# Optimization experiments

Hardware: AMD Instinct MI355X
Metric: run time of the kernel (lower is better)

## Reference

```python
import jax, jax.numpy as jnp
import numpy as np

KERNEL_MUL = 2.0
KERNEL_NUM = 5


def _mmd_channel(s, t):
    """Multi-bandwidth Gaussian-kernel MMD for one channel. s,t: [B, D]."""
    B = s.shape[0]
    total = jnp.concatenate([s, t], axis=0)            # [2B, D]
    sq = jnp.sum(total * total, axis=1)                # [2B]
    # ||xi - xj||^2 via Gram identity (avoids [2B,2B,D] intermediate)
    L2 = sq[:, None] + sq[None, :] - 2.0 * (total @ total.T)  # [2B, 2B]
    n = 2 * B
    # torch uses L2_distance.data -> bandwidth is detached
    bandwidth = jax.lax.stop_gradient(jnp.sum(L2)) / (n * n - n)
    bandwidth = bandwidth / (KERNEL_MUL ** (KERNEL_NUM // 2))
    bws = bandwidth * (KERNEL_MUL ** jnp.arange(KERNEL_NUM, dtype=s.dtype))  # [K_num]
    kernels = jnp.sum(jnp.exp(-L2[None, :, :] / bws[:, None, None]), axis=0)  # [2B, 2B]
    XX = kernels[:B, :B]
    YY = kernels[B:, B:]
    XY = kernels[:B, B:]
    YX = kernels[B:, :B]
    return jnp.mean(XX + YY - XY - YX)


def setup_inputs() -> dict:
    key = jax.random.key(0)
    k1, k2 = jax.random.split(key)
    B, K, H, W = 128, 21, 64, 64
    source = jax.random.normal(k1, (B, K, H, W), dtype=jnp.float32)
    target = jax.random.normal(k2, (B, K, H, W), dtype=jnp.float32)
    return {"source": source, "target": target}


def reference(source, target):
    B, K = source.shape[0], source.shape[1]
    s = source.reshape(B, K, -1)  # [B, K, D]
    t = target.reshape(B, K, -1)
    per_channel = jax.vmap(_mmd_channel, in_axes=(1, 1))(s, t)  # [K]
    return jnp.sum(per_channel) / K
```

## Files before the change

### kernel.cpp

```cpp
#include <hip/hip_runtime.h>
#include <hip/hip_bf16.h>
#include <stdint.h>

typedef __attribute__((ext_vector_type(4))) float f32x4;
typedef __attribute__((ext_vector_type(8))) short bf16x8;
typedef __attribute__((ext_vector_type(4))) uint32_t u32x4;

#define NCH 21
#define NROW 256
#define DIM 4096
#define BMP 128
#define BK 64
#define LDSS 72
#define NTILE 10

__device__ const int g_TI[NTILE] = {0, 0, 0, 0, 1, 1, 1, 2, 2, 3};
__device__ const int g_TJ[NTILE] = {0, 1, 2, 3, 1, 2, 3, 2, 3, 3};

__device__ __forceinline__ uint32_t pack_bf2(float x, float y) {
  __hip_bfloat162 h = __float22bfloat162_rn(float2{x, y});
  union { __hip_bfloat162 h; uint32_t u; } c;
  c.h = h;
  return c.u;
}

__global__ __launch_bounds__(512) void gram_kernel(
    const float* __restrict__ src, const float* __restrict__ tgt,
    float* __restrict__ Gp, int kshift, int kchunk) {
  const int P = 1 << kshift;
  const int NG = NCH << kshift;
  const int q = NG >> 3, r8 = NG & 7;
  const int x = blockIdx.x & 7;
  const int slot = blockIdx.x >> 3;
  const int cnt = q + (x < r8 ? 1 : 0);
  if (slot >= cnt * 3) return;
  const int gbase = (x < r8) ? x * (q + 1) : r8 * (q + 1) + (x - r8) * q;
  const int gi = slot / 3;
  const int bt = slot - gi * 3;
  const int g = gbase + gi;
  const int ch = g >> kshift;
  const int ks = g & (P - 1);
  const int kbase = ks * kchunk;
  const int row_base = (bt == 1) ? 128 : 0;
  const int col_base = (bt == 0) ? 0 : 128;
  const bool isdiag = (bt != 2);
  const int tid = threadIdx.x;
  const int lane = tid & 63;

  __shared__ __attribute__((aligned(16))) ushort As[BMP * LDSS];
  __shared__ __attribute__((aligned(16))) ushort Bs[BMP * LDSS];

  f32x4 acc[2][4];
#pragma unroll
  for (int m = 0; m < 2; ++m)
#pragma unroll
    for (int n = 0; n < 4; ++n)
      acc[m][n] = (f32x4){0.f, 0.f, 0.f, 0.f};

  const int wave = tid >> 6;
  const int wr = (wave >> 1) * 32;
  const int wc = (wave & 1) * 64;

  const int r0 = tid >> 3;
  const int c8 = (tid & 7) * 8;
  const float* Ab = row_base ? tgt : src;
  const float* Bb = col_base ? tgt : src;
  const float* ap[2];
  const float* bp[2];
#pragma unroll
  for (int p = 0; p < 2; ++p) {
    ap[p] = Ab + ((size_t)(r0 + p * 64) * NCH + ch) * DIM + c8;
    bp[p] = Bb + ((size_t)(r0 + p * 64) * NCH + ch) * DIM + c8;
  }

  f32x4 va[2][2], vb[2][2];
#pragma unroll
  for (int p = 0; p < 2; ++p) {
    va[p][0] = *reinterpret_cast<const f32x4*>(ap[p] + kbase);
    va[p][1] = *reinterpret_cast<const f32x4*>(ap[p] + kbase + 4);
    if (!isdiag) {
      vb[p][0] = *reinterpret_cast<const f32x4*>(bp[p] + kbase);
      vb[p][1] = *reinterpret_cast<const f32x4*>(bp[p] + kbase + 4);
    }
  }

  const int kend = kbase + kchunk;
  for (int k0 = kbase; k0 < kend; k0 += BK) {
    __syncthreads();
#pragma unroll
    for (int p = 0; p < 2; ++p) {
      u32x4 wa;
      wa.x = pack_bf2(va[p][0].x, va[p][0].y);
      wa.y = pack_bf2(va[p][0].z, va[p][0].w);
      wa.z = pack_bf2(va[p][1].x, va[p][1].y);
      wa.w = pack_bf2(va[p][1].z, va[p][1].w);
      *reinterpret_cast<u32x4*>(&As[(r0 + p * 64) * LDSS + c8]) = wa;
      if (!isdiag) {
        u32x4 wb;
        wb.x = pack_bf2(vb[p][0].x, vb[p][0].y);
        wb.y = pack_bf2(vb[p][0].z, vb[p][0].w);
        wb.z = pack_bf2(vb[p][1].x, vb[p][1].y);
        wb.w = pack_bf2(vb[p][1].z, vb[p][1].w);
        *reinterpret_cast<u32x4*>(&Bs[(r0 + p * 64) * LDSS + c8]) = wb;
      }
    }
    if (k0 + BK < kend) {
#pragma unroll
      for (int p = 0; p < 2; ++p) {
        va[p][0] = *reinterpret_cast<const f32x4*>(ap[p] + k0 + BK);
        va[p][1] = *reinterpret_cast<const f32x4*>(ap[p] + k0 + BK + 4);
        if (!isdiag) {
          vb[p][0] = *reinterpret_cast<const f32x4*>(bp[p] + k0 + BK);
          vb[p][1] = *reinterpret_cast<const f32x4*>(bp[p] + k0 + BK + 4);
        }
      }
    }
    asm volatile("s_waitcnt lgkmcnt(0)" ::: "memory");
    __builtin_amdgcn_s_barrier();
    asm volatile("" ::: "memory");

    const ushort* Bsrc = isdiag ? As : Bs;
#pragma unroll
    for (int kk = 0; kk < 2; ++kk) {
      const int kb = kk * 32 + (lane >> 4) * 8;
      bf16x8 a[2], b[4];
#pragma unroll
      for (int m = 0; m < 2; ++m)
        a[m] = *reinterpret_cast<const bf16x8*>(
            &As[(wr + m * 16 + (lane & 15)) * LDSS + kb]);
#pragma unroll
      for (int n = 0; n < 4; ++n)
        b[n] = *reinterpret_cast<const bf16x8*>(
            &Bsrc[(wc + n * 16 + (lane & 15)) * LDSS + kb]);
#pragma unroll
      for (int m = 0; m < 2; ++m)
#pragma unroll
        for (int n = 0; n < 4; ++n)
          acc[m][n] = __builtin_amdgcn_mfma_f32_16x16x32_bf16(a[m], b[n],
                                                              acc[m][n], 0, 0, 0);
    }
  }

  float* gp = Gp + (size_t)(ch * P + ks) * (NROW * NROW);
#pragma unroll
  for (int m = 0; m < 2; ++m)
#pragma unroll
    for (int n = 0; n < 4; ++n) {
      const int grow = row_base + wr + m * 16 + ((lane >> 4) << 2);
      const int gcol = col_base + wc + n * 16 + (lane & 15);
      if ((grow >> 6) > (gcol >> 6)) continue;
#pragma unroll
      for (int j = 0; j < 4; ++j)
        gp[(size_t)(grow + j) * NROW + gcol] = acc[m][n][j];
    }
}

__device__ __forceinline__ float block_sum256(float v, float* sm) {
#pragma unroll
  for (int o = 32; o > 0; o >>= 1) v += __shfl_down(v, o, 64);
  const int lane = threadIdx.x & 63;
  const int w = threadIdx.x >> 6;
  if (lane == 0) sm[w] = v;
  __syncthreads();
  float r = 0.f;
  if (threadIdx.x == 0) r = sm[0] + sm[1] + sm[2] + sm[3];
  __syncthreads();
  return r;
}

__global__ __launch_bounds__(256) void foldsum_kernel(
    const f32x4* __restrict__ Gp, f32x4* __restrict__ Gf,
    float* __restrict__ sums, int P) {
  const int t = blockIdx.x;
  const int ch = blockIdx.y;
  const int ti = g_TI[t], tj = g_TJ[t];
  const bool isdiag = (ti == tj);
  const int tid = threadIdx.x;
  float s = 0.f, tr = 0.f;
#pragma unroll
  for (int i = 0; i < 4; ++i) {
    const int idx4 = tid * 4 + i;
    const int rrow = idx4 >> 4;
    const int c4 = idx4 & 15;
    const int base_v = (ti * 64 + rrow) * 64 + tj * 16 + c4;
    f32x4 v = Gp[(size_t)(ch * P) * 16384 + base_v];
    for (int p = 1; p < P; ++p) v += Gp[(size_t)(ch * P + p) * 16384 + base_v];
    Gf[(size_t)ch * 16384 + base_v] = v;
    s += (v.x + v.y) + (v.z + v.w);
    if (isdiag) {
      const int cb = c4 * 4;
#pragma unroll
      for (int e = 0; e < 4; ++e)
        if (cb + e == rrow) tr += v[e];
    }
  }
  __shared__ float sm[4];
  float sG = block_sum256(s, sm);
  float sT = block_sum256(tr, sm);
  if (tid == 0) {
    sums[ch * 20 + t] = sG;
    if (isdiag) sums[ch * 20 + 10 + ti] = sT;
  }
}

__global__ __launch_bounds__(256) void mmd_kernel(const float* __restrict__ Gf,
                                                  const float* __restrict__ sums,
                                                  float* __restrict__ partial) {
  const int t = blockIdx.x;
  const int ch = blockIdx.y;
  const int ti = g_TI[t], tj = g_TJ[t];
  const int tid = threadIdx.x;
  const float* g = Gf + (size_t)ch * (NROW * NROW);

  const float* sc = sums + ch * 20;
  float sumG = 0.f;
#pragma unroll
  for (int k = 0; k < NTILE; ++k)
    sumG += (g_TI[k] == g_TJ[k] ? 1.f : 2.f) * sc[k];
  const float trace = (sc[10] + sc[11]) + (sc[12] + sc[13]);
  const float sumL2 = 2.f * NROW * trace - 2.f * sumG;
  const float bw = sumL2 / (float)(NROW * NROW - NROW) * 0.25f;
  float inv[5];
#pragma unroll
  for (int a = 0; a < 5; ++a) inv[a] = -1.f / (bw * (float)(1 << a));

  __shared__ float dA[64], dB[64];
  if (tid < 64) dA[tid] = g[(size_t)(ti * 64 + tid) * (NROW + 1)];
  else if (tid < 128) dB[tid - 64] = g[(size_t)(tj * 64 + (tid - 64)) * (NROW + 1)];
  __syncthreads();

  const int col = tid & 63;
  const int qq = tid >> 6;
  const float dj = dB[col];
  float acc = 0.f;
#pragma unroll 4
  for (int it = 0; it < 16; ++it) {
    const int r = it * 4 + qq;
    const float L2 = dA[r] + dj - 2.f * g[(size_t)(ti * 64 + r) * NROW + tj * 64 + col];
    float kv = 0.f;
#pragma unroll
    for (int a = 0; a < 5; ++a) kv += __expf(L2 * inv[a]);
    acc += kv;
  }
  __shared__ float sm[4];
  float tot = block_sum256(acc, sm);
  if (tid == 0) {
    float w = (ti == tj) ? 1.f : 2.f;
    float sgn = ((ti >= 2) == (tj >= 2)) ? 1.f : -1.f;
    partial[ch * NTILE + t] = tot * w * sgn;
  }
}

__global__ __launch_bounds__(256) void final_kernel(const float* __restrict__ partial,
                                                    float* __restrict__ out) {
  const int tid = threadIdx.x;
  float v = (tid < NCH * NTILE) ? partial[tid] : 0.f;
  __shared__ float sm[4];
  float tot = block_sum256(v, sm);
  if (tid == 0) out[0] = tot * (1.f / (NCH * 128.f * 128.f));
}

extern "C" void kernel_launch(void* const* d_in, const int* in_sizes, int n_in,
                              void* d_out, int out_size, void* d_ws, size_t ws_size,
                              hipStream_t stream) {
  const float* src = (const float*)d_in[0];
  const float* tgt = (const float*)d_in[1];
  float* out = (float*)d_out;
  const size_t GSZ = (size_t)NROW * NROW;

  int kshift = 0;
  if (ws_size >= (NCH * 9 * GSZ + 512) * sizeof(float)) kshift = 3;
  else if (ws_size >= (NCH * 5 * GSZ + 512) * sizeof(float)) kshift = 2;
  else if (ws_size >= (NCH * 3 * GSZ + 512) * sizeof(float)) kshift = 1;
  const int P = 1 << kshift;

  float* Gp = (float*)d_ws;
  float* Gf = (P > 1) ? Gp + (size_t)NCH * P * GSZ : Gp;
  float* sums = Gf + (size_t)NCH * GSZ;
  float* partial = sums + NCH * 20;

  const int NG = NCH * P;
  const int q = NG / 8, r8 = NG % 8;
  const int grid = 8 * (q + (r8 ? 1 : 0)) * 3;

  gram_kernel<<<dim3(grid), 512, 0, stream>>>(src, tgt, Gp, kshift, DIM >> kshift);
  foldsum_kernel<<<dim3(NTILE, NCH), 256, 0, stream>>>((const f32x4*)Gp,
                                                       (f32x4*)Gf, sums, P);
  mmd_kernel<<<dim3(NTILE, NCH), 256, 0, stream>>>(Gf, sums, partial);
  final_kernel<<<1, 256, 0, stream>>>(partial, out);
}
```

Baseline: 45.91 us.

## Double-buffer global prefetch registers and allow a 16-way K split

The Gram kernel's K loop is unrolled by two and keeps two register sets of prefetched fp32 data, so global loads are issued two BK steps ahead of the MFMA work that consumes them. The host also gains a kshift=4 option, splitting K into 16 chunks when the workspace is large enough, which raises block count but makes the fold-sum kernel read twice as many partial Gram matrices. The extra register buffers raise VGPR pressure. The loop assumes each K chunk holds an even number of BK steps, which holds for the chunk sizes in use.

```diff
diff --git a/kernel.cpp b/kernel.cpp
--- a/kernel.cpp
+++ b/kernel.cpp
@@ -22,6 +22,48 @@
   union { __hip_bfloat162 h; uint32_t u; } c;
   c.h = h;
   return c.u;
+}
+
+struct StageCtx {
+  const float* ap[2];
+  const float* bp[2];
+  bool isdiag;
+  int r0, c8, kend;
+};
+
+__device__ __forceinline__ void fill_slot(const StageCtx& cx, f32x4 (&va)[2][2],
+                                          f32x4 (&vb)[2][2], int k) {
+#pragma unroll
+  for (int p = 0; p < 2; ++p) {
+    va[p][0] = *reinterpret_cast<const f32x4*>(cx.ap[p] + k);
+    va[p][1] = *reinterpret_cast<const f32x4*>(cx.ap[p] + k + 4);
+    if (!cx.isdiag) {
+      vb[p][0] = *reinterpret_cast<const f32x4*>(cx.bp[p] + k);
+      vb[p][1] = *reinterpret_cast<const f32x4*>(cx.bp[p] + k + 4);
+    }
+  }
+}
+
+__device__ __forceinline__ void stage_slot(const StageCtx& cx, ushort* As,
+                                           ushort* Bs, f32x4 (&va)[2][2],
+                                           f32x4 (&vb)[2][2]) {
+#pragma unroll
+  for (int p = 0; p < 2; ++p) {
+    u32x4 wa;
+    wa.x = pack_bf2(va[p][0].x, va[p][0].y);
+    wa.y = pack_bf2(va[p][0].z, va[p][0].w);
+    wa.z = pack_bf2(va[p][1].x, va[p][1].y);
+    wa.w = pack_bf2(va[p][1].z, va[p][1].w);
+    *reinterpret_cast<u32x4*>(&As[(cx.r0 + p * 64) * LDSS + cx.c8]) = wa;
+    if (!cx.isdiag) {
+      u32x4 wb;
+      wb.x = pack_bf2(vb[p][0].x, vb[p][0].y);
+      wb.y = pack_bf2(vb[p][0].z, vb[p][0].w);
+      wb.z = pack_bf2(vb[p][1].x, vb[p][1].y);
+      wb.w = pack_bf2(vb[p][1].z, vb[p][1].w);
+      *reinterpret_cast<u32x4*>(&Bs[(cx.r0 + p * 64) * LDSS + cx.c8]) = wb;
+    }
+  }
 }
 
 __global__ __launch_bounds__(512) void gram_kernel(
@@ -43,7 +85,6 @@
   const int kbase = ks * kchunk;
   const int row_base = (bt == 1) ? 128 : 0;
   const int col_base = (bt == 0) ? 0 : 128;
-  const bool isdiag = (bt != 2);
   const int tid = threadIdx.x;
   const int lane = tid & 63;
 
@@ -61,83 +102,86 @@
   const int wr = (wave >> 1) * 32;
   const int wc = (wave & 1) * 64;
 
-  const int r0 = tid >> 3;
-  const int c8 = (tid & 7) * 8;
-  const float* Ab = row_base ? tgt : src;
-  const float* Bb = col_base ? tgt : src;
-  const float* ap[2];
-  const float* bp[2];
-#pragma unroll
-  for (int p = 0; p < 2; ++p) {
-    ap[p] = Ab + ((size_t)(r0 + p * 64) * NCH + ch) * DIM + c8;
-    bp[p] = Bb + ((size_t)(r0 + p * 64) * NCH + ch) * DIM + c8;
-  }
-
-  f32x4 va[2][2], vb[2][2];
-#pragma unroll
-  for (int p = 0; p < 2; ++p) {
-    va[p][0] = *reinterpret_cast<const f32x4*>(ap[p] + kbase);
-    va[p][1] = *reinterpret_cast<const f32x4*>(ap[p] + kbase + 4);
-    if (!isdiag) {
-      vb[p][0] = *reinterpret_cast<const f32x4*>(bp[p] + kbase);
-      vb[p][1] = *reinterpret_cast<const f32x4*>(bp[p] + kbase + 4);
-    }
-  }
-
-  const int kend = kbase + kchunk;
-  for (int k0 = kbase; k0 < kend; k0 += BK) {
-    __syncthreads();
+  StageCtx cx;
+  cx.isdiag = (bt != 2);
+  cx.r0 = tid >> 3;
+  cx.c8 = (tid & 7) * 8;
+  cx.kend = kbase + kchunk;
+  {
+    const float* Ab = row_base ? tgt : src;
+    const float* Bb = col_base ? tgt : src;
 #pragma unroll
     for (int p = 0; p < 2; ++p) {
-      u32x4 wa;
-      wa.x = pack_bf2(va[p][0].x, va[p][0].y);
-      wa.y = pack_bf2(va[p][0].z, va[p][0].w);
-      wa.z = pack_bf2(va[p][1].x, va[p][1].y);
-      wa.w = pack_bf2(va[p][1].z, va[p][1].w);
-      *reinterpret_cast<u32x4*>(&As[(r0 + p * 64) * LDSS + c8]) = wa;
-      if (!isdiag) {
-        u32x4 wb;
-        wb.x = pack_bf2(vb[p][0].x, vb[p][0].y);
-        wb.y = pack_bf2(vb[p][0].z, vb[p][0].w);
-        wb.z = pack_bf2(vb[p][1].x, vb[p][1].y);
-        wb.w = pack_bf2(vb[p][1].z, vb[p][1].w);
-        *reinterpret_cast<u32x4*>(&Bs[(r0 + p * 64) * LDSS + c8]) = wb;
-      }
-    }
-    if (k0 + BK < kend) {
-#pragma unroll
-      for (int p = 0; p < 2; ++p) {
-        va[p][0] = *reinterpret_cast<const f32x4*>(ap[p] + k0 + BK);
-        va[p][1] = *reinterpret_cast<const f32x4*>(ap[p] + k0 + BK + 4);
-        if (!isdiag) {
-          vb[p][0] = *reinterpret_cast<const f32x4*>(bp[p] + k0 + BK);
-          vb[p][1] = *reinterpret_cast<const f32x4*>(bp[p] + k0 + BK + 4);
-        }
-      }
-    }
+      cx.ap[p] = Ab + ((size_t)(cx.r0 + p * 64) * NCH + ch) * DIM + cx.c8;
+      cx.bp[p] = Bb + ((size_t)(cx.r0 + p * 64) * NCH + ch) * DIM + cx.c8;
+    }
+  }
+
+  f32x4 vaA[2][2], vbA[2][2], vaB[2][2], vbB[2][2];
+  fill_slot(cx, vaA, vbA, kbase);
+  fill_slot(cx, vaB, vbB, kbase + BK);
+
+  for (int k0 = kbase; k0 < cx.kend; k0 += 2 * BK) {
+    asm volatile("s_waitcnt lgkmcnt(0)" ::: "memory");
+    __builtin_amdgcn_s_barrier();
+    stage_slot(cx, As, Bs, vaA, vbA);
+    if (k0 + 2 * BK < cx.kend) fill_slot(cx, vaA, vbA, k0 + 2 * BK);
     asm volatile("s_waitcnt lgkmcnt(0)" ::: "memory");
     __builtin_amdgcn_s_barrier();
     asm volatile("" ::: "memory");
 
-    const ushort* Bsrc = isdiag ? As : Bs;
-#pragma unroll
-    for (int kk = 0; kk < 2; ++kk) {
-      const int kb = kk * 32 + (lane >> 4) * 8;
-      bf16x8 a[2], b[4];
-#pragma unroll
-      for (int m = 0; m < 2; ++m)
-        a[m] = *reinterpret_cast<const bf16x8*>(
-            &As[(wr + m * 16 + (lane & 15)) * LDSS + kb]);
-#pragma unroll
-      for (int n = 0; n < 4; ++n)
-        b[n] = *reinterpret_cast<const bf16x8*>(
-            &Bsrc[(wc + n * 16 + (lane & 15)) * LDSS + kb]);
-#pragma unroll
-      for (int m = 0; m < 2; ++m)
+    {
+      const ushort* Bsrc = cx.isdiag ? As : Bs;
+#pragma unroll
+      for (int kk = 0; kk < 2; ++kk) {
+        const int kb = kk * 32 + (lane >> 4) * 8;
+        bf16x8 a[2], b[4];
+#pragma unroll
+        for (int m = 0; m < 2; ++m)
+          a[m] = *reinterpret_cast<const bf16x8*>(
+              &As[(wr + m * 16 + (lane & 15)) * LDSS + kb]);
 #pragma unroll
         for (int n = 0; n < 4; ++n)
-          acc[m][n] = __builtin_amdgcn_mfma_f32_16x16x32_bf16(a[m], b[n],
-                                                              acc[m][n], 0, 0, 0);
+          b[n] = *reinterpret_cast<const bf16x8*>(
+              &Bsrc[(wc + n * 16 + (lane & 15)) * LDSS + kb]);
+#pragma unroll
+        for (int m = 0; m < 2; ++m)
+#pragma unroll
+          for (int n = 0; n < 4; ++n)
+            acc[m][n] = __builtin_amdgcn_mfma_f32_16x16x32_bf16(a[m], b[n],
+                                                                acc[m][n], 0, 0, 0);
+      }
+    }
+
+    asm volatile("s_waitcnt lgkmcnt(0)" ::: "memory");
+    __builtin_amdgcn_s_barrier();
+    stage_slot(cx, As, Bs, vaB, vbB);
+    if (k0 + 3 * BK < cx.kend) fill_slot(cx, vaB, vbB, k0 + 3 * BK);
+    asm volatile("s_waitcnt lgkmcnt(0)" ::: "memory");
+    __builtin_amdgcn_s_barrier();
+    asm volatile("" ::: "memory");
+
+    {
+      const ushort* Bsrc = cx.isdiag ? As : Bs;
+#pragma unroll
+      for (int kk = 0; kk < 2; ++kk) {
+        const int kb = kk * 32 + (lane >> 4) * 8;
+        bf16x8 a[2], b[4];
+#pragma unroll
+        for (int m = 0; m < 2; ++m)
+          a[m] = *reinterpret_cast<const bf16x8*>(
+              &As[(wr + m * 16 + (lane & 15)) * LDSS + kb]);
+#pragma unroll
+        for (int n = 0; n < 4; ++n)
+          b[n] = *reinterpret_cast<const bf16x8*>(
+              &Bsrc[(wc + n * 16 + (lane & 15)) * LDSS + kb]);
+#pragma unroll
+        for (int m = 0; m < 2; ++m)
+#pragma unroll
+          for (int n = 0; n < 4; ++n)
+            acc[m][n] = __builtin_amdgcn_mfma_f32_16x16x32_bf16(a[m], b[n],
+                                                                acc[m][n], 0, 0, 0);
+      }
     }
   }
 
@@ -269,7 +313,8 @@
   const size_t GSZ = (size_t)NROW * NROW;
 
   int kshift = 0;
-  if (ws_size >= (NCH * 9 * GSZ + 512) * sizeof(float)) kshift = 3;
+  if (ws_size >= (NCH * 17 * GSZ + 512) * sizeof(float)) kshift = 4;
+  else if (ws_size >= (NCH * 9 * GSZ + 512) * sizeof(float)) kshift = 3;
   else if (ws_size >= (NCH * 5 * GSZ + 512) * sizeof(float)) kshift = 2;
   else if (ws_size >= (NCH * 3 * GSZ + 512) * sizeof(float)) kshift = 1;
   const int P = 1 << kshift;
```

Result: slower. 83.61 us (+82.1%).

## Restructure gram kernel global loads: wider BK, row-contiguous wave loads, no prefetch

Applied to the files above, without the earlier changes.

The gram kernel now uses a K-tile of 128 instead of 64. Each wave loads 16 rows, with 32 lanes covering a contiguous 512-byte span of one row, so every load instruction issues 8 independent float4 loads per operand. The register-prefetch double buffering is replaced by load-then-store within each iteration, with a barrier added at the end of each iteration, and a launch-bounds occupancy hint is added. The goal is better global coalescing and more memory parallelism per instruction with fewer barriers per unit of K. The cost is losing overlap of global loads with MFMA work, and the LDS footprint roughly doubles, which may limit occupancy.

```diff
diff --git a/kernel.cpp b/kernel.cpp
--- a/kernel.cpp
+++ b/kernel.cpp
@@ -4,14 +4,12 @@
 
 typedef __attribute__((ext_vector_type(4))) float f32x4;
 typedef __attribute__((ext_vector_type(8))) short bf16x8;
-typedef __attribute__((ext_vector_type(4))) uint32_t u32x4;
 
 #define NCH 21
 #define NROW 256
 #define DIM 4096
-#define BMP 128
-#define BK 64
-#define LDSS 72
+#define BK 128
+#define LDSS2 132
 #define NTILE 10
 
 __device__ const int g_TI[NTILE] = {0, 0, 0, 0, 1, 1, 1, 2, 2, 3};
@@ -24,7 +22,7 @@
   return c.u;
 }
 
-__global__ __launch_bounds__(512) void gram_kernel(
+__global__ __launch_bounds__(512, 4) void gram_kernel(
     const float* __restrict__ src, const float* __restrict__ tgt,
     float* __restrict__ Gp, int kshift, int kchunk) {
   const int P = 1 << kshift;
@@ -46,9 +44,10 @@
   const bool isdiag = (bt != 2);
   const int tid = threadIdx.x;
   const int lane = tid & 63;
-
-  __shared__ __attribute__((aligned(16))) ushort As[BMP * LDSS];
-  __shared__ __attribute__((aligned(16))) ushort Bs[BMP * LDSS];
+  const int w = tid >> 6;
+
+  __shared__ __attribute__((aligned(16))) ushort As[128 * LDSS2];
+  __shared__ __attribute__((aligned(16))) ushort Bs[128 * LDSS2];
 
   f32x4 acc[2][4];
 #pragma unroll
@@ -57,62 +56,46 @@
     for (int n = 0; n < 4; ++n)
       acc[m][n] = (f32x4){0.f, 0.f, 0.f, 0.f};
 
-  const int wave = tid >> 6;
-  const int wr = (wave >> 1) * 32;
-  const int wc = (wave & 1) * 64;
-
-  const int r0 = tid >> 3;
-  const int c8 = (tid & 7) * 8;
+  const int wr = (w >> 1) * 32;
+  const int wc = (w & 1) * 64;
+
+  const int subrow = lane >> 5;
+  const int kf = (lane & 31) * 4;
   const float* Ab = row_base ? tgt : src;
   const float* Bb = col_base ? tgt : src;
-  const float* ap[2];
-  const float* bp[2];
-#pragma unroll
-  for (int p = 0; p < 2; ++p) {
-    ap[p] = Ab + ((size_t)(r0 + p * 64) * NCH + ch) * DIM + c8;
-    bp[p] = Bb + ((size_t)(r0 + p * 64) * NCH + ch) * DIM + c8;
-  }
-
-  f32x4 va[2][2], vb[2][2];
-#pragma unroll
-  for (int p = 0; p < 2; ++p) {
-    va[p][0] = *reinterpret_cast<const f32x4*>(ap[p] + kbase);
-    va[p][1] = *reinterpret_cast<const f32x4*>(ap[p] + kbase + 4);
+  const float* apr[8];
+  const float* bpr[8];
+#pragma unroll
+  for (int p = 0; p < 8; ++p) {
+    const int row = w * 16 + 2 * p + subrow;
+    apr[p] = Ab + ((size_t)row * NCH + ch) * DIM + kbase + kf;
+    bpr[p] = Bb + ((size_t)row * NCH + ch) * DIM + kbase + kf;
+  }
+  const int lw0 = (w * 16 + subrow) * LDSS2 + kf;
+
+  const int nk = kchunk / BK;
+
+  for (int it = 0; it < nk; ++it) {
+    const int ko = it * BK;
+    f32x4 v[8];
+#pragma unroll
+    for (int p = 0; p < 8; ++p) v[p] = *reinterpret_cast<const f32x4*>(apr[p] + ko);
+#pragma unroll
+    for (int p = 0; p < 8; ++p) {
+      uint2 wv;
+      wv.x = pack_bf2(v[p].x, v[p].y);
+      wv.y = pack_bf2(v[p].z, v[p].w);
+      *reinterpret_cast<uint2*>(&As[lw0 + 2 * p * LDSS2]) = wv;
+    }
     if (!isdiag) {
-      vb[p][0] = *reinterpret_cast<const f32x4*>(bp[p] + kbase);
-      vb[p][1] = *reinterpret_cast<const f32x4*>(bp[p] + kbase + 4);
-    }
-  }
-
-  const int kend = kbase + kchunk;
-  for (int k0 = kbase; k0 < kend; k0 += BK) {
-    __syncthreads();
-#pragma unroll
-    for (int p = 0; p < 2; ++p) {
-      u32x4 wa;
-      wa.x = pack_bf2(va[p][0].x, va[p][0].y);
-      wa.y = pack_bf2(va[p][0].z, va[p][0].w);
-      wa.z = pack_bf2(va[p][1].x, va[p][1].y);
-      wa.w = pack_bf2(va[p][1].z, va[p][1].w);
-      *reinterpret_cast<u32x4*>(&As[(r0 + p * 64) * LDSS + c8]) = wa;
-      if (!isdiag) {
-        u32x4 wb;
-        wb.x = pack_bf2(vb[p][0].x, vb[p][0].y);
-        wb.y = pack_bf2(vb[p][0].z, vb[p][0].w);
-        wb.z = pack_bf2(vb[p][1].x, vb[p][1].y);
-        wb.w = pack_bf2(vb[p][1].z, vb[p][1].w);
-        *reinterpret_cast<u32x4*>(&Bs[(r0 + p * 64) * LDSS + c8]) = wb;
-      }
-    }
-    if (k0 + BK < kend) {
-#pragma unroll
-      for (int p = 0; p < 2; ++p) {
-        va[p][0] = *reinterpret_cast<const f32x4*>(ap[p] + k0 + BK);
-        va[p][1] = *reinterpret_cast<const f32x4*>(ap[p] + k0 + BK + 4);
-        if (!isdiag) {
-          vb[p][0] = *reinterpret_cast<const f32x4*>(bp[p] + k0 + BK);
-          vb[p][1] = *reinterpret_cast<const f32x4*>(bp[p] + k0 + BK + 4);
-        }
+#pragma unroll
+      for (int p = 0; p < 8; ++p) v[p] = *reinterpret_cast<const f32x4*>(bpr[p] + ko);
+#pragma unroll
+      for (int p = 0; p < 8; ++p) {
+        uint2 wv;
+        wv.x = pack_bf2(v[p].x, v[p].y);
+        wv.y = pack_bf2(v[p].z, v[p].w);
+        *reinterpret_cast<uint2*>(&Bs[lw0 + 2 * p * LDSS2]) = wv;
       }
     }
     asm volatile("s_waitcnt lgkmcnt(0)" ::: "memory");
@@ -121,17 +104,17 @@
 
     const ushort* Bsrc = isdiag ? As : Bs;
 #pragma unroll
-    for (int kk = 0; kk < 2; ++kk) {
+    for (int kk = 0; kk < 4; ++kk) {
       const int kb = kk * 32 + (lane >> 4) * 8;
       bf16x8 a[2], b[4];
 #pragma unroll
       for (int m = 0; m < 2; ++m)
         a[m] = *reinterpret_cast<const bf16x8*>(
-            &As[(wr + m * 16 + (lane & 15)) * LDSS + kb]);
+            &As[(wr + m * 16 + (lane & 15)) * LDSS2 + kb]);
 #pragma unroll
       for (int n = 0; n < 4; ++n)
         b[n] = *reinterpret_cast<const bf16x8*>(
-            &Bsrc[(wc + n * 16 + (lane & 15)) * LDSS + kb]);
+            &Bsrc[(wc + n * 16 + (lane & 15)) * LDSS2 + kb]);
 #pragma unroll
       for (int m = 0; m < 2; ++m)
 #pragma unroll
@@ -139,6 +122,9 @@
           acc[m][n] = __builtin_amdgcn_mfma_f32_16x16x32_bf16(a[m], b[n],
                                                               acc[m][n], 0, 0, 0);
     }
+    asm volatile("s_waitcnt lgkmcnt(0)" ::: "memory");
+    __builtin_amdgcn_s_barrier();
+    asm volatile("" ::: "memory");
   }
 
   float* gp = Gp + (size_t)(ch * P + ks) * (NROW * NROW);
@@ -159,8 +145,8 @@
 #pragma unroll
   for (int o = 32; o > 0; o >>= 1) v += __shfl_down(v, o, 64);
   const int lane = threadIdx.x & 63;
-  const int w = threadIdx.x >> 6;
-  if (lane == 0) sm[w] = v;
+  const int wv = threadIdx.x >> 6;
+  if (lane == 0) sm[wv] = v;
   __syncthreads();
   float r = 0.f;
   if (threadIdx.x == 0) r = sm[0] + sm[1] + sm[2] + sm[3];
@@ -210,7 +196,7 @@
   const int ch = blockIdx.y;
   const int ti = g_TI[t], tj = g_TJ[t];
   const int tid = threadIdx.x;
-  const float* g = Gf + (size_t)ch * (NROW * NROW);
+  const float* gg = Gf + (size_t)ch * (NROW * NROW);
 
   const float* sc = sums + ch * 20;
   float sumG = 0.f;
@@ -225,8 +211,8 @@
   for (int a = 0; a < 5; ++a) inv[a] = -1.f / (bw * (float)(1 << a));
 
   __shared__ float dA[64], dB[64];
-  if (tid < 64) dA[tid] = g[(size_t)(ti * 64 + tid) * (NROW + 1)];
-  else if (tid < 128) dB[tid - 64] = g[(size_t)(tj * 64 + (tid - 64)) * (NROW + 1)];
+  if (tid < 64) dA[tid] = gg[(size_t)(ti * 64 + tid) * (NROW + 1)];
+  else if (tid < 128) dB[tid - 64] = gg[(size_t)(tj * 64 + (tid - 64)) * (NROW + 1)];
   __syncthreads();
 
   const int col = tid & 63;
@@ -236,7 +222,7 @@
 #pragma unroll 4
   for (int it = 0; it < 16; ++it) {
     const int r = it * 4 + qq;
-    const float L2 = dA[r] + dj - 2.f * g[(size_t)(ti * 64 + r) * NROW + tj * 64 + col];
+    const float L2 = dA[r] + dj - 2.f * gg[(size_t)(ti * 64 + r) * NROW + tj * 64 + col];
     float kv = 0.f;
 #pragma unroll
     for (int a = 0; a < 5; ++a) kv += __expf(L2 * inv[a]);
@@ -245,9 +231,9 @@
   __shared__ float sm[4];
   float tot = block_sum256(acc, sm);
   if (tid == 0) {
-    float w = (ti == tj) ? 1.f : 2.f;
+    float wgt = (ti == tj) ? 1.f : 2.f;
     float sgn = ((ti >= 2) == (tj >= 2)) ? 1.f : -1.f;
-    partial[ch * NTILE + t] = tot * w * sgn;
+    partial[ch * NTILE + t] = tot * wgt * sgn;
   }
 }
 
```

Result: slower. 68.18 us (+48.5%).
